# Performance work log

Measured on AMD Instinct MI355X. Metric: run time of the kernel, lower is better.

The kernel has to match this reference:

```python
import jax, jax.numpy as jnp
import numpy as np

B, N, ACHAN, VCHAN, H = 1, 2048, 128, 64, 8
KQ_ADIM, KQ_VDIM = 32, 16
AVALDIM, VVALDIM = ACHAN // H, VCHAN // H
KQ_PRESCALE, KQ_SCALE = 0.01, 0.1
R0_LIST = [0.5, 1.0, 2.0, 4.0, 0.5, 1.0, 2.0, 4.0]


def _init_w(key, shape, scale=1.0):
    # matches _param_init_with_scale: std = scale * fan_in**-0.5, shape (H, fan_in, fan_out)
    std = scale * shape[1] ** (-0.5)
    return std * jax.random.normal(key, shape, dtype=jnp.float32)


def setup_inputs() -> dict:
    key = jax.random.key(0)
    ks = jax.random.split(key, 12)
    kq_ascale = (KQ_PRESCALE / KQ_ADIM) ** 0.5
    kq_vscale = (KQ_PRESCALE / KQ_VDIM) ** 0.5
    return {
        "ax": jax.random.normal(ks[0], (B, N, ACHAN), jnp.float32),
        "vx": jax.random.normal(ks[1], (B, N, VCHAN, 3), jnp.float32),
        "pos_k": jax.random.normal(ks[2], (B, N, 3), jnp.float32),
        "pos_q": jax.random.normal(ks[3], (B, N, 3), jnp.float32),
        "r0": jnp.array(R0_LIST, jnp.float32),
        "W_ak": _init_w(ks[4], (H, KQ_ADIM, ACHAN), kq_ascale),
        "W_vk": _init_w(ks[5], (H, KQ_VDIM, VCHAN), kq_vscale),
        "W_aq": _init_w(ks[6], (H, KQ_ADIM, ACHAN), kq_ascale),
        "W_vq": _init_w(ks[7], (H, KQ_VDIM, VCHAN), kq_vscale),
        "W_aval": _init_w(ks[8], (H, AVALDIM, ACHAN)),
        "W_vval": _init_w(ks[9], (H, VVALDIM, VCHAN)),
        "W_a2vval": _init_w(ks[10], (H, VVALDIM, ACHAN)),
        "W_v2aval": _init_w(ks[11], (H, AVALDIM, VCHAN)),
    }


def reference(ax, vx, pos_k, pos_q, r0, W_ak, W_vk, W_aq, W_vq, W_aval, W_vval, W_a2vval, W_v2aval):
    batch, nodes, achan = ax.shape
    vchan = vx.shape[2]
    # key/query projections per head
    ak = jnp.einsum('hij,bnj->bnhi', W_ak, ax)      # (b,n,h,kq_adim)
    vk = jnp.einsum('hij,bnjv->bnhiv', W_vk, vx)    # (b,n,h,kq_vdim,3)
    aq = jnp.einsum('hij,bnj->bnhi', W_aq, ax)
    vq = jnp.einsum('hij,bnjv->bnhiv', W_vq, vx)
    akq_dot = jnp.einsum('bnhi,bmhi->bnmh', ak, aq)
    vkq_dot = jnp.einsum('bnhiv,bmhiv->bnmh', vk, vq)
    dot = KQ_SCALE * (akq_dot + vkq_dot)            # (b,n,m,h)
    # spatial proximity bias
    separation = pos_k[:, None, :, :] - pos_q[:, :, None, :]   # (b,n,m,3)
    dist_sq = jnp.sum(separation ** 2, axis=3)                 # (b,n,m)
    r0_sq = r0 ** 2
    proximity = r0_sq / (r0_sq + dist_sq[..., None])           # (b,n,m,h)
    directions = separation[:, :, :, None, :] * jnp.sqrt(proximity / r0_sq)[..., None]  # (b,n,m,h,3)
    attention = jax.nn.softmax(dot + jnp.log(proximity), axis=1)  # softmax over keys n
    # value mixing (project values per node first, then attend)
    aval = jnp.einsum('hij,bnj->bnhi', W_aval, ax)              # (b,n,h,avaldim)
    vval = jnp.einsum('hij,bnjv->bnhiv', W_vval, vx)            # (b,n,h,vvaldim,3)
    aans = jnp.einsum('bnmh,bnhi->bmhi', attention, aval)
    vans = jnp.einsum('bnmh,bnhiv->bmhiv', attention, vval)
    v2a = jnp.einsum('hij,bnjv->bnhiv', W_v2aval, vx)           # (b,n,h,avaldim,3)
    a2v = jnp.einsum('hij,bnj->bnhi', W_a2vval, ax)             # (b,n,h,vvaldim)
    aans = aans + jnp.einsum('bnmh,bnhiv,bnmhv->bmhi', attention, v2a, directions)
    vans = vans + jnp.einsum('bnmh,bnhi,bnmhv->bmhiv', attention, a2v, directions)
    return (aans.reshape(batch, nodes, achan), vans.reshape(batch, nodes, vchan, 3))
```

## Files before the change

### kernel.cpp

```cpp
#include <hip/hip_runtime.h>

#define NN 2048
#define NH 8

typedef __attribute__((ext_vector_type(4))) short s4;
typedef __attribute__((ext_vector_type(8))) short s8;
typedef __attribute__((ext_vector_type(4))) float f4;

static __device__ __forceinline__ ushort f2b(float x) {
    uint u = __builtin_bit_cast(uint, x);
    uint r = (u + 0x7FFFu + ((u >> 16) & 1u)) >> 16;
    return (ushort)r;
}
static __device__ __forceinline__ float b2f(ushort b) {
    return __builtin_bit_cast(float, ((uint)b) << 16);
}
static __device__ __forceinline__ uint pu(ushort a, ushort b) {
    return (uint)a | ((uint)b << 16);
}
static __device__ __forceinline__ s4 pack4(float a, float b, float c, float d) {
    uint2 w; w.x = pu(f2b(a), f2b(b)); w.y = pu(f2b(c), f2b(d));
    return __builtin_bit_cast(s4, w);
}
static __device__ __forceinline__ f4 mfma32(s8 a, s8 b, f4 c) {
    return __builtin_amdgcn_mfma_f32_16x16x32_bf16(a, b, c, 0, 0, 0);
}
static __device__ __forceinline__ f4 mfma16(s4 a, s4 b, f4 c) {
    const s4 z4s = {0, 0, 0, 0};
    s8 a8 = __builtin_shufflevector(a, z4s, 0, 1, 2, 3, 4, 5, 6, 7);
    s8 b8 = __builtin_shufflevector(b, z4s, 0, 1, 2, 3, 4, 5, 6, 7);
    return __builtin_amdgcn_mfma_f32_16x16x32_bf16(a8, b8, c, 0, 0, 0);
}

__global__ __launch_bounds__(256) void proj_kernel(
    const float* __restrict__ ax, const float* __restrict__ vx,
    const float* __restrict__ W_ak, const float* __restrict__ W_vk,
    const float* __restrict__ W_aq, const float* __restrict__ W_vq,
    const float* __restrict__ W_aval, const float* __restrict__ W_vval,
    const float* __restrict__ W_a2vval, const float* __restrict__ W_v2aval,
    ushort* __restrict__ Kf, ushort* __restrict__ Qf, ushort* __restrict__ Vn)
{
    __shared__ float axs[8][128];
    __shared__ float vxs[3][8][64];
    __shared__ __align__(16) ushort kqs[2][8][8][80];
    __shared__ __align__(16) ushort vns[8][8][152];
    const int t  = threadIdx.x;
    const int n0 = blockIdx.x * 8;

    for (int idx = t; idx < 8 * 128; idx += 256)
        axs[idx >> 7][idx & 127] = ax[n0 * 128 + idx];
    for (int idx = t; idx < 8 * 192; idx += 256) {
        int nb = idx / 192, r = idx - nb * 192;
        int j = r / 3, v = r - j * 3;
        vxs[v][nb][j] = vx[n0 * 192 + idx];
    }
    __syncthreads();

    #pragma unroll 1
    for (int rr = 0; rr < 8; ++rr) {
        int r = rr * 256 + t;
        const float* wrow; int h, v = 0, col = 0, vrow = -1, dsti = 0; bool isA;
        float scale = 1.0f;
        if (r < 256)       { int q = r;        h = q >> 5; wrow = W_ak     + q * 128;               isA = true;  dsti = 0; col = q & 31; }
        else if (r < 512)  { int q = r - 256;  h = q >> 5; wrow = W_aq     + q * 128;               isA = true;  dsti = 1; col = q & 31; scale = 0.1f; }
        else if (r < 896)  { int q = r - 512;  h = q / 48; int s = q - h * 48; v = s % 3; wrow = W_vk     + (h * 16 + s / 3) * 64; isA = false; dsti = 0; col = 32 + s; }
        else if (r < 1280) { int q = r - 896;  h = q / 48; int s = q - h * 48; v = s % 3; wrow = W_vq     + (h * 16 + s / 3) * 64; isA = false; dsti = 1; col = 32 + s; scale = 0.1f; }
        else if (r < 1408) { int q = r - 1280; h = q >> 4; wrow = W_aval   + q * 128;               isA = true;  vrow = q & 15; }
        else if (r < 1600) { int q = r - 1408; h = q / 24; int s = q - h * 24; v = s % 3; wrow = W_vval   + (h * 8  + s / 3) * 64; isA = false; vrow = 16 + s; }
        else if (r < 1984) { int q = r - 1600; h = q / 48; int s = q - h * 48; v = s % 3; wrow = W_v2aval + (h * 16 + s / 3) * 64; isA = false; vrow = 48 + s; }
        else               { int q = r - 1984; h = q >> 3; wrow = W_a2vval + q * 128;               isA = true;  vrow = 112 + (q & 7); }

        float acc[8] = {0.f, 0.f, 0.f, 0.f, 0.f, 0.f, 0.f, 0.f};
        if (isA) {
            for (int j = 0; j < 128; j += 4) {
                float4 w4 = *(const float4*)(wrow + j);
                #pragma unroll
                for (int nb = 0; nb < 8; ++nb) {
                    float4 x4 = *(const float4*)(&axs[nb][j]);
                    acc[nb] += w4.x * x4.x + w4.y * x4.y + w4.z * x4.z + w4.w * x4.w;
                }
            }
        } else {
            for (int j = 0; j < 64; j += 4) {
                float4 w4 = *(const float4*)(wrow + j);
                #pragma unroll
                for (int nb = 0; nb < 8; ++nb) {
                    float4 x4 = *(const float4*)(&vxs[v][nb][j]);
                    acc[nb] += w4.x * x4.x + w4.y * x4.y + w4.z * x4.z + w4.w * x4.w;
                }
            }
        }
        #pragma unroll
        for (int nb = 0; nb < 8; ++nb) {
            ushort bv = f2b(scale * acc[nb]);
            if (vrow >= 0) vns[h][nb][vrow] = bv;
            else           kqs[dsti][nb][h][col] = bv;
        }
    }
    __syncthreads();

    for (int i = t; i < 1280; i += 256) {
        int dsti = i / 640, rem = i - dsti * 640;
        int row = rem / 10, part = rem - row * 10;
        int h = row >> 3, nb = row & 7;
        uint4 val = *(const uint4*)(&kqs[dsti][nb][h][part * 8]);
        ushort* g = (dsti ? Qf : Kf) + ((size_t)h * NN + n0 + nb) * 128 + part * 8;
        *(uint4*)g = val;
    }
    for (int i = t; i < 1216; i += 256) {
        int row = i / 19, part = i - row * 19;
        int h = row >> 3, nb = row & 7;
        uint4 val = *(const uint4*)(&vns[h][nb][part * 8]);
        *(uint4*)(Vn + ((size_t)h * NN + n0 + nb) * 152 + part * 8) = val;
    }
}

__global__ __launch_bounds__(256) void finish_kernel(
    const float* __restrict__ pos_k, const float* __restrict__ pos_q,
    ushort* __restrict__ Kf, ushort* __restrict__ Qf)
{
    int g = blockIdx.x * 256 + threadIdx.x;
    int h = g >> 11, n = g & 2047;
    float pqx = pos_q[n * 3], pqy = pos_q[n * 3 + 1], pqz = pos_q[n * 3 + 2];
    float pkx = pos_k[n * 3], pky = pos_k[n * 3 + 1], pkz = pos_k[n * 3 + 2];

    ushort phx = f2b(pqx), phy = f2b(pqy), phz = f2b(pqz);
    float sq = pqx * pqx + pqy * pqy + pqz * pqz;
    ushort sqh = f2b(sq);
    ushort thx = f2b(pkx), thy = f2b(pky), thz = f2b(pkz);
    ushort qhx = f2b(-2.0f * b2f(thx)), qhy = f2b(-2.0f * b2f(thy)), qhz = f2b(-2.0f * b2f(thz));
    float sk = pkx * pkx + pky * pky + pkz * pkz;
    ushort skh = f2b(sk);

    uint4 z4; z4.x = 0; z4.y = 0; z4.z = 0; z4.w = 0;
    uint4 ka0, ka1;
    ka0.x = pu(phx, f2b(pqx - b2f(phx)));
    ka0.y = pu(phx, phy);
    ka0.z = pu(f2b(pqy - b2f(phy)), phy);
    ka0.w = pu(phz, f2b(pqz - b2f(phz)));
    ka1.x = pu(phz, sqh);
    ka1.y = pu(f2b(sq - b2f(sqh)), 0x3F80);
    ka1.z = pu(0x3F80, 0);
    ka1.w = 0;
    uint4 qa0, qa1;
    qa0.x = pu(qhx, qhx);
    qa0.y = pu(f2b(-2.0f * (pkx - b2f(thx))), qhy);
    qa0.z = pu(qhy, f2b(-2.0f * (pky - b2f(thy))));
    qa0.w = pu(qhz, qhz);
    qa1.x = pu(f2b(-2.0f * (pkz - b2f(thz))), 0x3F80);
    qa1.y = pu(0x3F80, skh);
    qa1.z = pu(f2b(sk - b2f(skh)), 0);
    qa1.w = 0;

    ushort* Ko = Kf + ((size_t)h * NN + n) * 128;
    ushort* Qo = Qf + ((size_t)h * NN + n) * 128;
    *(uint4*)(Ko + 80) = z4;  *(uint4*)(Ko + 88) = z4;
    *(uint4*)(Ko + 96) = ka0; *(uint4*)(Ko + 104) = ka1;
    *(uint4*)(Ko + 112) = z4; *(uint4*)(Ko + 120) = z4;
    *(uint4*)(Qo + 80) = z4;  *(uint4*)(Qo + 88) = z4;
    *(uint4*)(Qo + 96) = qa0; *(uint4*)(Qo + 104) = qa1;
    *(uint4*)(Qo + 112) = z4; *(uint4*)(Qo + 120) = z4;
}

__global__ __launch_bounds__(256) void vtrans_kernel(
    const ushort* __restrict__ Vn, const float* __restrict__ pos_q,
    ushort* __restrict__ Vt)
{
    __shared__ ushort lds_n[64 * 160];
    __shared__ float lds_pq[192];
    const int bid = blockIdx.x;
    const int h = bid & 7, n0 = (bid >> 3) * 64;
    const int t = threadIdx.x;

    const ushort* src = Vn + ((size_t)h * NN + n0) * 152;
    #pragma unroll
    for (int p = 0; p < 5; ++p) {
        int idx = p * 256 + t;
        if (idx < 1216) {
            int node = idx / 19, ch = idx - node * 19;
            *(uint4*)(&lds_n[node * 160 + ch * 8]) =
                *(const uint4*)(src + (size_t)node * 152 + ch * 8);
        }
    }
    if (t < 192) lds_pq[t] = pos_q[n0 * 3 + t];
    __syncthreads();

    #pragma unroll 1
    for (int p = 0; p < 5; ++p) {
        int fi = p * 32 + (t >> 3);
        if (fi < 144) {
            int nb0 = (t & 7) * 8;
            uint rr[4];
            #pragma unroll
            for (int e = 0; e < 8; ++e) {
                int node = nb0 + e;
                const ushort* row = lds_n + node * 160;
                ushort bv;
                if (fi < 40 || (fi >= 48 && fi < 96) || (fi >= 112 && fi < 120)) {
                    bv = row[fi];
                } else if (fi < 48) {
                    bv = (fi == 40) ? (ushort)0x3F80 : (ushort)0;
                } else if (fi < 112) {
                    int i = fi - 96;
                    float val = b2f(row[48 + 3 * i]) * lds_pq[node * 3 + 0]
                              + b2f(row[49 + 3 * i]) * lds_pq[node * 3 + 1]
                              + b2f(row[50 + 3 * i]) * lds_pq[node * 3 + 2];
                    bv = f2b(val);
                } else {
                    int s = fi - 120, ip = s / 3, v = s - 3 * ip;
                    bv = f2b(b2f(row[112 + ip]) * lds_pq[node * 3 + v]);
                }
                if ((e & 1) == 0) rr[e >> 1] = bv;
                else              rr[e >> 1] |= ((uint)bv) << 16;
            }
            uint4 outw; outw.x = rr[0]; outw.y = rr[1]; outw.z = rr[2]; outw.w = rr[3];
            *(uint4*)(Vt + ((size_t)h * 144 + fi) * NN + n0 + nb0) = outw;
        }
    }
}

__global__ __launch_bounds__(256, 2) void attn_kernel(
    const ushort* __restrict__ Kf, const ushort* __restrict__ Qf,
    const ushort* __restrict__ Vt, const float* __restrict__ pos_k,
    const float* __restrict__ r0, float* __restrict__ out)
{
    __shared__ __align__(16) char smem[39168];
    const int bid = blockIdx.x;
    const int h = bid & 7;
    const int m0 = (bid >> 3) * 32;
    const int t = threadIdx.x;
    const int lane = t & 63, w = t >> 6;
    const int l15 = lane & 15, lg = lane >> 4;
    const int kh = w >> 1, qh = w & 1;

    const float r0h = r0[h], r0sq = r0h * r0h;
    const ushort* Kg = Kf + (size_t)h * NN * 128;
    const ushort* Vg = Vt + (size_t)h * 144 * NN;

    const ushort* Qp = Qf + ((size_t)h * NN + m0 + qh * 16 + l15) * 128 + lg * 8;
    const s8 qb0 = *(const s8*)(Qp);
    const s8 qb1 = *(const s8*)(Qp + 32);
    const s8 qb2 = *(const s8*)(Qp + 64);
    const s8 qb3 = *(const s8*)(Qp + 96);

    f4 acc[9];
    #pragma unroll
    for (int jb = 0; jb < 9; ++jb) acc[jb] = (f4){0.f, 0.f, 0.f, 0.f};

    uint4 kreg0, kreg1, vreg0, vreg1, vreg2;
    const int kt = t >> 4, kgr = t & 15;
    const int vf = t >> 2, vg = t & 3;
    const int kc = kgr * 8;
    const int vc = vg * 8;
    const int kS = (((kgr & 8) | ((kgr + kt) & 7))) << 4;
    const int kws0 = kt * 256 + kS;
    const int kws1 = kws0 + 4096;
    const int vS = ((vg + (vf >> 1)) & 3) << 4;
    const int vws0 = vf * 64 + vS;
    const int vws1 = vws0 + 4096;
    const int vws2 = vws0 + 8192;

    const int kro = (kh * 16 + l15) * 256;
    const int e0 = ((lg + l15) & 7) << 4;
    const int e1 = ((lg + l15 + 4) & 7) << 4;
    const int vxo = (((kh * 2 + (lg >> 1) + (l15 >> 1)) & 3) << 4) + ((lg & 1) << 3);

#define LOAD_TILE(k0)                                                               \
    kreg0 = *(const uint4*)(Kg + (size_t)((k0) + kt) * 128 + kc);                   \
    kreg1 = *(const uint4*)(Kg + (size_t)((k0) + 16 + kt) * 128 + kc);              \
    vreg0 = *(const uint4*)(Vg + (size_t)vf * NN + (k0) + vc);                      \
    vreg1 = *(const uint4*)(Vg + (size_t)(vf + 64) * NN + (k0) + vc);               \
    if (t < 64) vreg2 = *(const uint4*)(Vg + (size_t)(vf + 128) * NN + (k0) + vc);

#define WRITE_TILE(b)                                                               \
  { char* kb_ = smem + (b) * 17408; char* vb_ = kb_ + 8192;                         \
    *(uint4*)(kb_ + kws0) = kreg0;  *(uint4*)(kb_ + kws1) = kreg1;                  \
    *(uint4*)(vb_ + vws0) = vreg0;  *(uint4*)(vb_ + vws1) = vreg1;                  \
    if (t < 64) *(uint4*)(vb_ + vws2) = vreg2; }

#define COMPUTE_TILE(b)                                                             \
  { const char* kb_ = smem + (b) * 17408; const char* vb_ = kb_ + 8192;             \
    const char* kr = kb_ + kro;                                                     \
    s8 ka0 = *(const s8*)(kr + e0);                                                 \
    s8 ka1 = *(const s8*)(kr + e1);                                                 \
    s8 ka2 = *(const s8*)(kr + 128 + e0);                                           \
    s8 ka3 = *(const s8*)(kr + 128 + e1);                                           \
    f4 z = (f4){0.f, 0.f, 0.f, 0.f};                                                \
    f4 dt = mfma32(ka0, qb0, z);                                                    \
    dt = mfma32(ka1, qb1, dt);                                                      \
    dt = mfma32(ka2, qb2, dt);                                                      \
    f4 dd = mfma32(ka3, qb3, z);                                                    \
    float pv[4], gv[4];                                                             \
    _Pragma("unroll")                                                               \
    for (int r = 0; r < 4; ++r) {                                                   \
      float x = r0sq + dd[r];                                                       \
      float rs = __builtin_amdgcn_rsqf(x);                                          \
      float tt = rs * rs;                                                           \
      float y = dt[r];                                                              \
      float e = fmaf(y, fmaf(0.5f, y, 1.0f), 1.0f);                                 \
      pv[r] = r0sq * tt * e;                                                        \
      gv[r] = pv[r] * rs;                                                           \
    }                                                                               \
    s4 pb = pack4(pv[0], pv[1], pv[2], pv[3]);                                      \
    s4 gb = pack4(gv[0], gv[1], gv[2], gv[3]);                                      \
    const char* vr = vb_ + l15 * 64 + vxo;                                          \
    _Pragma("unroll")                                                               \
    for (int jb = 0; jb < 3; ++jb)                                                  \
      acc[jb] = mfma16(*(const s4*)(vr + jb * 1024), pb, acc[jb]);                  \
    _Pragma("unroll")                                                               \
    for (int jb = 3; jb < 9; ++jb)                                                  \
      acc[jb] = mfma16(*(const s4*)(vr + jb * 1024), gb, acc[jb]);                  \
  }

    LOAD_TILE(0)
    WRITE_TILE(0)
    __syncthreads();
    #pragma unroll 2
    for (int tile = 0; tile < 64; ++tile) {
        int b = tile & 1;
        if (tile < 63) { LOAD_TILE((tile + 1) * 32) }
        COMPUTE_TILE(b)
        __syncthreads();
        if (tile < 63) { WRITE_TILE(b ^ 1) }
        __syncthreads();
    }

    float* smemf = (float*)smem;
    float my[36];
    #pragma unroll
    for (int jb = 0; jb < 9; ++jb)
        #pragma unroll
        for (int r = 0; r < 4; ++r)
            my[jb * 4 + r] = acc[jb][r];

    if (w >= 2) {
        float* p = smemf + ((w - 2) * 64 + lane) * 37;
        #pragma unroll
        for (int i = 0; i < 36; ++i) p[i] = my[i];
    }
    __syncthreads();
    if (w < 2) {
        const float* p = smemf + (w * 64 + lane) * 37;
        #pragma unroll
        for (int i = 0; i < 36; ++i) my[i] += p[i];
    }
    __syncthreads();
    if (w < 2) {
        #pragma unroll
        for (int jb = 0; jb < 9; ++jb)
            #pragma unroll
            for (int r = 0; r < 4; ++r)
                smemf[((size_t)w * 144 + jb * 16 + lg * 4 + r) * 17 + l15]
                    = my[jb * 4 + r];
    }
    __syncthreads();

    {
        int q = t & 31, task = t >> 5;
        int m = m0 + q, qh2 = q >> 4, ml = q & 15;
        const float* R = smemf + (size_t)qh2 * 144 * 17 + ml;
        float inv = 1.0f / R[40 * 17];
        float pk0 = pos_k[m * 3], pk1 = pos_k[m * 3 + 1], pk2 = pos_k[m * 3 + 2];
        #pragma unroll
        for (int oo = 0; oo < 5; ++oo) {
            int o = task * 5 + oo;
            if (o < 16) {
                int i = o;
                float val = R[i * 17] + pk0 * R[(48 + 3 * i) * 17] + pk1 * R[(49 + 3 * i) * 17]
                          + pk2 * R[(50 + 3 * i) * 17] - R[(96 + i) * 17];
                out[(size_t)m * 128 + h * 16 + i] = val * inv;
            } else {
                int s = o - 16, ip = s / 3, v3 = s - 3 * ip;
                float pkv = (v3 == 0) ? pk0 : ((v3 == 1) ? pk1 : pk2);
                float val = R[(16 + s) * 17] + pkv * R[(112 + ip) * 17] - R[(120 + s) * 17];
                out[(size_t)NN * 128 + (size_t)m * 192 + h * 24 + s] = val * inv;
            }
        }
    }
#undef LOAD_TILE
#undef WRITE_TILE
#undef COMPUTE_TILE
}

extern "C" void kernel_launch(void* const* d_in, const int* in_sizes, int n_in,
                              void* d_out, int out_size, void* d_ws, size_t ws_size,
                              hipStream_t stream) {
    const float* ax       = (const float*)d_in[0];
    const float* vx       = (const float*)d_in[1];
    const float* pos_k    = (const float*)d_in[2];
    const float* pos_q    = (const float*)d_in[3];
    const float* r0       = (const float*)d_in[4];
    const float* W_ak     = (const float*)d_in[5];
    const float* W_vk     = (const float*)d_in[6];
    const float* W_aq     = (const float*)d_in[7];
    const float* W_vq     = (const float*)d_in[8];
    const float* W_aval   = (const float*)d_in[9];
    const float* W_vval   = (const float*)d_in[10];
    const float* W_a2vval = (const float*)d_in[11];
    const float* W_v2aval = (const float*)d_in[12];

    ushort* Kf = (ushort*)d_ws;
    ushort* Qf = Kf + (size_t)NH * NN * 128;
    ushort* Vn = Qf + (size_t)NH * NN * 128;
    ushort* Vt = Vn + (size_t)NH * NN * 152;
    float*  outp = (float*)d_out;

    hipLaunchKernelGGL(proj_kernel, dim3(NN / 8), dim3(256), 0, stream,
                       ax, vx, W_ak, W_vk, W_aq, W_vq, W_aval, W_vval,
                       W_a2vval, W_v2aval, Kf, Qf, Vn);
    hipLaunchKernelGGL(finish_kernel, dim3(64), dim3(256), 0, stream,
                       pos_k, pos_q, Kf, Qf);
    hipLaunchKernelGGL(vtrans_kernel, dim3(32 * NH), dim3(256), 0, stream,
                       Vn, pos_q, Vt);
    hipLaunchKernelGGL(attn_kernel, dim3(64 * NH), dim3(256), 0, stream,
                       Kf, Qf, Vt, pos_k, r0, outp);
}
```

Baseline: 111.5 us.

## Fuse position finish and value transpose into projection kernel

Merges finish_kernel and vtrans_kernel into proj_kernel, so four launches become two. The value rows are now written directly in the transposed Vt layout. The position-weighted terms are computed from a pos_q-contracted vx in shared memory and from scaled a2v rows, which removes the Vn intermediate buffer and its round trip through global memory. The block size doubles to 512 threads. The projection does slightly more work (2368 rows instead of 2048), and each thread writes 16-byte chunks strided across Vt rows.

```diff
diff --git a/kernel.cpp b/kernel.cpp
--- a/kernel.cpp
+++ b/kernel.cpp
@@ -18,8 +18,11 @@
 static __device__ __forceinline__ uint pu(ushort a, ushort b) {
     return (uint)a | ((uint)b << 16);
 }
+static __device__ __forceinline__ uint bpack(float lo, float hi) {
+    return pu(f2b(lo), f2b(hi));
+}
 static __device__ __forceinline__ s4 pack4(float a, float b, float c, float d) {
-    uint2 w; w.x = pu(f2b(a), f2b(b)); w.y = pu(f2b(c), f2b(d));
+    uint2 w; w.x = bpack(a, b); w.y = bpack(c, d);
     return __builtin_bit_cast(s4, w);
 }
 static __device__ __forceinline__ f4 mfma32(s8 a, s8 b, f4 c) {
@@ -32,46 +35,58 @@
     return __builtin_amdgcn_mfma_f32_16x16x32_bf16(a8, b8, c, 0, 0, 0);
 }
 
-__global__ __launch_bounds__(256) void proj_kernel(
+__global__ __launch_bounds__(512) void proj_kernel(
     const float* __restrict__ ax, const float* __restrict__ vx,
+    const float* __restrict__ pos_k, const float* __restrict__ pos_q,
     const float* __restrict__ W_ak, const float* __restrict__ W_vk,
     const float* __restrict__ W_aq, const float* __restrict__ W_vq,
     const float* __restrict__ W_aval, const float* __restrict__ W_vval,
     const float* __restrict__ W_a2vval, const float* __restrict__ W_v2aval,
-    ushort* __restrict__ Kf, ushort* __restrict__ Qf, ushort* __restrict__ Vn)
+    ushort* __restrict__ Kf, ushort* __restrict__ Qf, ushort* __restrict__ Vt)
 {
     __shared__ float axs[8][128];
     __shared__ float vxs[3][8][64];
+    __shared__ float xts[8][64];
+    __shared__ float pqs[8][3];
     __shared__ __align__(16) ushort kqs[2][8][8][80];
-    __shared__ __align__(16) ushort vns[8][8][152];
     const int t  = threadIdx.x;
     const int n0 = blockIdx.x * 8;
 
-    for (int idx = t; idx < 8 * 128; idx += 256)
+    for (int idx = t; idx < 1024; idx += 512)
         axs[idx >> 7][idx & 127] = ax[n0 * 128 + idx];
-    for (int idx = t; idx < 8 * 192; idx += 256) {
+    for (int idx = t; idx < 1536; idx += 512) {
         int nb = idx / 192, r = idx - nb * 192;
         int j = r / 3, v = r - j * 3;
         vxs[v][nb][j] = vx[n0 * 192 + idx];
     }
+    if (t < 24) pqs[t / 3][t % 3] = pos_q[n0 * 3 + t];
+    __syncthreads();
+    {
+        int nb = t >> 6, j = t & 63;
+        xts[nb][j] = vxs[0][nb][j] * pqs[nb][0] + vxs[1][nb][j] * pqs[nb][1]
+                   + vxs[2][nb][j] * pqs[nb][2];
+    }
     __syncthreads();
 
     #pragma unroll 1
-    for (int rr = 0; rr < 8; ++rr) {
-        int r = rr * 256 + t;
-        const float* wrow; int h, v = 0, col = 0, vrow = -1, dsti = 0; bool isA;
+    for (int rr = 0; rr < 5; ++rr) {
+        int r = rr * 512 + t;
+        if (r >= 2368) continue;
+        const float* wrow; int h, v = 0, col = -1, vrow = -1, dsti = 0, srcT = 0, pv = -1;
         float scale = 1.0f;
-        if (r < 256)       { int q = r;        h = q >> 5; wrow = W_ak     + q * 128;               isA = true;  dsti = 0; col = q & 31; }
-        else if (r < 512)  { int q = r - 256;  h = q >> 5; wrow = W_aq     + q * 128;               isA = true;  dsti = 1; col = q & 31; scale = 0.1f; }
-        else if (r < 896)  { int q = r - 512;  h = q / 48; int s = q - h * 48; v = s % 3; wrow = W_vk     + (h * 16 + s / 3) * 64; isA = false; dsti = 0; col = 32 + s; }
-        else if (r < 1280) { int q = r - 896;  h = q / 48; int s = q - h * 48; v = s % 3; wrow = W_vq     + (h * 16 + s / 3) * 64; isA = false; dsti = 1; col = 32 + s; scale = 0.1f; }
-        else if (r < 1408) { int q = r - 1280; h = q >> 4; wrow = W_aval   + q * 128;               isA = true;  vrow = q & 15; }
-        else if (r < 1600) { int q = r - 1408; h = q / 24; int s = q - h * 24; v = s % 3; wrow = W_vval   + (h * 8  + s / 3) * 64; isA = false; vrow = 16 + s; }
-        else if (r < 1984) { int q = r - 1600; h = q / 48; int s = q - h * 48; v = s % 3; wrow = W_v2aval + (h * 16 + s / 3) * 64; isA = false; vrow = 48 + s; }
-        else               { int q = r - 1984; h = q >> 3; wrow = W_a2vval + q * 128;               isA = true;  vrow = 112 + (q & 7); }
+        if (r < 256)       { int q = r;        h = q >> 5; wrow = W_ak + q * 128; srcT = 0; col = q & 31; dsti = 0; }
+        else if (r < 512)  { int q = r - 256;  h = q >> 5; wrow = W_aq + q * 128; srcT = 0; col = q & 31; dsti = 1; scale = 0.1f; }
+        else if (r < 896)  { int q = r - 512;  h = q / 48; int s = q - h * 48; v = s % 3; wrow = W_vk + (h * 16 + s / 3) * 64; srcT = 1; col = 32 + s; dsti = 0; }
+        else if (r < 1280) { int q = r - 896;  h = q / 48; int s = q - h * 48; v = s % 3; wrow = W_vq + (h * 16 + s / 3) * 64; srcT = 1; col = 32 + s; dsti = 1; scale = 0.1f; }
+        else if (r < 1408) { int q = r - 1280; h = q >> 4; wrow = W_aval + q * 128; srcT = 0; vrow = q & 15; }
+        else if (r < 1600) { int q = r - 1408; h = q / 24; int s = q - h * 24; v = s % 3; wrow = W_vval + (h * 8 + s / 3) * 64; srcT = 1; vrow = 16 + s; }
+        else if (r < 1984) { int q = r - 1600; h = q / 48; int s = q - h * 48; v = s % 3; wrow = W_v2aval + (h * 16 + s / 3) * 64; srcT = 1; vrow = 48 + s; }
+        else if (r < 2048) { int q = r - 1984; h = q >> 3; wrow = W_a2vval + q * 128; srcT = 0; vrow = 112 + (q & 7); }
+        else if (r < 2176) { int q = r - 2048; h = q >> 4; wrow = W_v2aval + (h * 16 + (q & 15)) * 64; srcT = 2; vrow = 96 + (q & 15); }
+        else               { int q = r - 2176; h = q / 24; int s = q - h * 24; int i = s / 3; pv = s % 3; wrow = W_a2vval + (h * 8 + i) * 128; srcT = 0; vrow = 120 + s; }
 
         float acc[8] = {0.f, 0.f, 0.f, 0.f, 0.f, 0.f, 0.f, 0.f};
-        if (isA) {
+        if (srcT == 0) {
             for (int j = 0; j < 128; j += 4) {
                 float4 w4 = *(const float4*)(wrow + j);
                 #pragma unroll
@@ -81,25 +96,34 @@
                 }
             }
         } else {
+            const float* sp = (srcT == 1) ? &vxs[v][0][0] : &xts[0][0];
             for (int j = 0; j < 64; j += 4) {
                 float4 w4 = *(const float4*)(wrow + j);
                 #pragma unroll
                 for (int nb = 0; nb < 8; ++nb) {
-                    float4 x4 = *(const float4*)(&vxs[v][nb][j]);
+                    float4 x4 = *(const float4*)(sp + nb * 64 + j);
                     acc[nb] += w4.x * x4.x + w4.y * x4.y + w4.z * x4.z + w4.w * x4.w;
                 }
             }
         }
-        #pragma unroll
-        for (int nb = 0; nb < 8; ++nb) {
-            ushort bv = f2b(scale * acc[nb]);
-            if (vrow >= 0) vns[h][nb][vrow] = bv;
-            else           kqs[dsti][nb][h][col] = bv;
+        if (vrow >= 0) {
+            float o[8];
+            #pragma unroll
+            for (int nb = 0; nb < 8; ++nb)
+                o[nb] = acc[nb] * (pv >= 0 ? pqs[nb][pv] : 1.0f);
+            uint4 pk;
+            pk.x = bpack(o[0], o[1]); pk.y = bpack(o[2], o[3]);
+            pk.z = bpack(o[4], o[5]); pk.w = bpack(o[6], o[7]);
+            *(uint4*)(Vt + ((size_t)(h * 144 + vrow)) * NN + n0) = pk;
+        } else {
+            #pragma unroll
+            for (int nb = 0; nb < 8; ++nb)
+                kqs[dsti][nb][h][col] = f2b(scale * acc[nb]);
         }
     }
     __syncthreads();
 
-    for (int i = t; i < 1280; i += 256) {
+    for (int i = t; i < 1280; i += 512) {
         int dsti = i / 640, rem = i - dsti * 640;
         int row = rem / 10, part = rem - row * 10;
         int h = row >> 3, nb = row & 7;
@@ -107,115 +131,54 @@
         ushort* g = (dsti ? Qf : Kf) + ((size_t)h * NN + n0 + nb) * 128 + part * 8;
         *(uint4*)g = val;
     }
-    for (int i = t; i < 1216; i += 256) {
-        int row = i / 19, part = i - row * 19;
-        int h = row >> 3, nb = row & 7;
-        uint4 val = *(const uint4*)(&vns[h][nb][part * 8]);
-        *(uint4*)(Vn + ((size_t)h * NN + n0 + nb) * 152 + part * 8) = val;
-    }
-}
-
-__global__ __launch_bounds__(256) void finish_kernel(
-    const float* __restrict__ pos_k, const float* __restrict__ pos_q,
-    ushort* __restrict__ Kf, ushort* __restrict__ Qf)
-{
-    int g = blockIdx.x * 256 + threadIdx.x;
-    int h = g >> 11, n = g & 2047;
-    float pqx = pos_q[n * 3], pqy = pos_q[n * 3 + 1], pqz = pos_q[n * 3 + 2];
-    float pkx = pos_k[n * 3], pky = pos_k[n * 3 + 1], pkz = pos_k[n * 3 + 2];
-
-    ushort phx = f2b(pqx), phy = f2b(pqy), phz = f2b(pqz);
-    float sq = pqx * pqx + pqy * pqy + pqz * pqz;
-    ushort sqh = f2b(sq);
-    ushort thx = f2b(pkx), thy = f2b(pky), thz = f2b(pkz);
-    ushort qhx = f2b(-2.0f * b2f(thx)), qhy = f2b(-2.0f * b2f(thy)), qhz = f2b(-2.0f * b2f(thz));
-    float sk = pkx * pkx + pky * pky + pkz * pkz;
-    ushort skh = f2b(sk);
-
-    uint4 z4; z4.x = 0; z4.y = 0; z4.z = 0; z4.w = 0;
-    uint4 ka0, ka1;
-    ka0.x = pu(phx, f2b(pqx - b2f(phx)));
-    ka0.y = pu(phx, phy);
-    ka0.z = pu(f2b(pqy - b2f(phy)), phy);
-    ka0.w = pu(phz, f2b(pqz - b2f(phz)));
-    ka1.x = pu(phz, sqh);
-    ka1.y = pu(f2b(sq - b2f(sqh)), 0x3F80);
-    ka1.z = pu(0x3F80, 0);
-    ka1.w = 0;
-    uint4 qa0, qa1;
-    qa0.x = pu(qhx, qhx);
-    qa0.y = pu(f2b(-2.0f * (pkx - b2f(thx))), qhy);
-    qa0.z = pu(qhy, f2b(-2.0f * (pky - b2f(thy))));
-    qa0.w = pu(qhz, qhz);
-    qa1.x = pu(f2b(-2.0f * (pkz - b2f(thz))), 0x3F80);
-    qa1.y = pu(0x3F80, skh);
-    qa1.z = pu(f2b(sk - b2f(skh)), 0);
-    qa1.w = 0;
-
-    ushort* Ko = Kf + ((size_t)h * NN + n) * 128;
-    ushort* Qo = Qf + ((size_t)h * NN + n) * 128;
-    *(uint4*)(Ko + 80) = z4;  *(uint4*)(Ko + 88) = z4;
-    *(uint4*)(Ko + 96) = ka0; *(uint4*)(Ko + 104) = ka1;
-    *(uint4*)(Ko + 112) = z4; *(uint4*)(Ko + 120) = z4;
-    *(uint4*)(Qo + 80) = z4;  *(uint4*)(Qo + 88) = z4;
-    *(uint4*)(Qo + 96) = qa0; *(uint4*)(Qo + 104) = qa1;
-    *(uint4*)(Qo + 112) = z4; *(uint4*)(Qo + 120) = z4;
-}
-
-__global__ __launch_bounds__(256) void vtrans_kernel(
-    const ushort* __restrict__ Vn, const float* __restrict__ pos_q,
-    ushort* __restrict__ Vt)
-{
-    __shared__ ushort lds_n[64 * 160];
-    __shared__ float lds_pq[192];
-    const int bid = blockIdx.x;
-    const int h = bid & 7, n0 = (bid >> 3) * 64;
-    const int t = threadIdx.x;
-
-    const ushort* src = Vn + ((size_t)h * NN + n0) * 152;
-    #pragma unroll
-    for (int p = 0; p < 5; ++p) {
-        int idx = p * 256 + t;
-        if (idx < 1216) {
-            int node = idx / 19, ch = idx - node * 19;
-            *(uint4*)(&lds_n[node * 160 + ch * 8]) =
-                *(const uint4*)(src + (size_t)node * 152 + ch * 8);
-        }
-    }
-    if (t < 192) lds_pq[t] = pos_q[n0 * 3 + t];
-    __syncthreads();
-
-    #pragma unroll 1
-    for (int p = 0; p < 5; ++p) {
-        int fi = p * 32 + (t >> 3);
-        if (fi < 144) {
-            int nb0 = (t & 7) * 8;
-            uint rr[4];
-            #pragma unroll
-            for (int e = 0; e < 8; ++e) {
-                int node = nb0 + e;
-                const ushort* row = lds_n + node * 160;
-                ushort bv;
-                if (fi < 40 || (fi >= 48 && fi < 96) || (fi >= 112 && fi < 120)) {
-                    bv = row[fi];
-                } else if (fi < 48) {
-                    bv = (fi == 40) ? (ushort)0x3F80 : (ushort)0;
-                } else if (fi < 112) {
-                    int i = fi - 96;
-                    float val = b2f(row[48 + 3 * i]) * lds_pq[node * 3 + 0]
-                              + b2f(row[49 + 3 * i]) * lds_pq[node * 3 + 1]
-                              + b2f(row[50 + 3 * i]) * lds_pq[node * 3 + 2];
-                    bv = f2b(val);
-                } else {
-                    int s = fi - 120, ip = s / 3, v = s - 3 * ip;
-                    bv = f2b(b2f(row[112 + ip]) * lds_pq[node * 3 + v]);
-                }
-                if ((e & 1) == 0) rr[e >> 1] = bv;
-                else              rr[e >> 1] |= ((uint)bv) << 16;
-            }
-            uint4 outw; outw.x = rr[0]; outw.y = rr[1]; outw.z = rr[2]; outw.w = rr[3];
-            *(uint4*)(Vt + ((size_t)h * 144 + fi) * NN + n0 + nb0) = outw;
-        }
+
+    if (t < 64) {
+        int h = t >> 3, nb = t & 7, n = n0 + nb;
+        float pqx = pqs[nb][0], pqy = pqs[nb][1], pqz = pqs[nb][2];
+        float pkx = pos_k[n * 3], pky = pos_k[n * 3 + 1], pkz = pos_k[n * 3 + 2];
+
+        ushort phx = f2b(pqx), phy = f2b(pqy), phz = f2b(pqz);
+        float sq = pqx * pqx + pqy * pqy + pqz * pqz;
+        ushort sqh = f2b(sq);
+        ushort thx = f2b(pkx), thy = f2b(pky), thz = f2b(pkz);
+        ushort qhx = f2b(-2.0f * b2f(thx)), qhy = f2b(-2.0f * b2f(thy)), qhz = f2b(-2.0f * b2f(thz));
+        float sk = pkx * pkx + pky * pky + pkz * pkz;
+        ushort skh = f2b(sk);
+
+        uint4 z4; z4.x = 0; z4.y = 0; z4.z = 0; z4.w = 0;
+        uint4 ka0, ka1;
+        ka0.x = pu(phx, f2b(pqx - b2f(phx)));
+        ka0.y = pu(phx, phy);
+        ka0.z = pu(f2b(pqy - b2f(phy)), phy);
+        ka0.w = pu(phz, f2b(pqz - b2f(phz)));
+        ka1.x = pu(phz, sqh);
+        ka1.y = pu(f2b(sq - b2f(sqh)), 0x3F80);
+        ka1.z = pu(0x3F80, 0);
+        ka1.w = 0;
+        uint4 qa0, qa1;
+        qa0.x = pu(qhx, qhx);
+        qa0.y = pu(f2b(-2.0f * (pkx - b2f(thx))), qhy);
+        qa0.z = pu(qhy, f2b(-2.0f * (pky - b2f(thy))));
+        qa0.w = pu(qhz, qhz);
+        qa1.x = pu(f2b(-2.0f * (pkz - b2f(thz))), 0x3F80);
+        qa1.y = pu(0x3F80, skh);
+        qa1.z = pu(f2b(sk - b2f(skh)), 0);
+        qa1.w = 0;
+
+        ushort* Ko = Kf + ((size_t)h * NN + n) * 128;
+        ushort* Qo = Qf + ((size_t)h * NN + n) * 128;
+        *(uint4*)(Ko + 80) = z4;  *(uint4*)(Ko + 88) = z4;
+        *(uint4*)(Ko + 96) = ka0; *(uint4*)(Ko + 104) = ka1;
+        *(uint4*)(Ko + 112) = z4; *(uint4*)(Ko + 120) = z4;
+        *(uint4*)(Qo + 80) = z4;  *(uint4*)(Qo + 88) = z4;
+        *(uint4*)(Qo + 96) = qa0; *(uint4*)(Qo + 104) = qa1;
+        *(uint4*)(Qo + 112) = z4; *(uint4*)(Qo + 120) = z4;
+    } else if (t < 128) {
+        int idx = t - 64, h = idx >> 3, rw = 40 + (idx & 7);
+        uint4 cv;
+        if (rw == 40) { cv.x = 0x3F803F80u; cv.y = 0x3F803F80u; cv.z = 0x3F803F80u; cv.w = 0x3F803F80u; }
+        else          { cv.x = 0; cv.y = 0; cv.z = 0; cv.w = 0; }
+        *(uint4*)(Vt + ((size_t)(h * 144 + rw)) * NN + n0) = cv;
     }
 }
 
@@ -401,17 +364,12 @@
 
     ushort* Kf = (ushort*)d_ws;
     ushort* Qf = Kf + (size_t)NH * NN * 128;
-    ushort* Vn = Qf + (size_t)NH * NN * 128;
-    ushort* Vt = Vn + (size_t)NH * NN * 152;
+    ushort* Vt = Qf + (size_t)NH * NN * 128;
     float*  outp = (float*)d_out;
 
-    hipLaunchKernelGGL(proj_kernel, dim3(NN / 8), dim3(256), 0, stream,
-                       ax, vx, W_ak, W_vk, W_aq, W_vq, W_aval, W_vval,
-                       W_a2vval, W_v2aval, Kf, Qf, Vn);
-    hipLaunchKernelGGL(finish_kernel, dim3(64), dim3(256), 0, stream,
-                       pos_k, pos_q, Kf, Qf);
-    hipLaunchKernelGGL(vtrans_kernel, dim3(32 * NH), dim3(256), 0, stream,
-                       Vn, pos_q, Vt);
+    hipLaunchKernelGGL(proj_kernel, dim3(NN / 8), dim3(512), 0, stream,
+                       ax, vx, pos_k, pos_q, W_ak, W_vk, W_aq, W_vq,
+                       W_aval, W_vval, W_a2vval, W_v2aval, Kf, Qf, Vt);
     hipLaunchKernelGGL(attn_kernel, dim3(64 * NH), dim3(256), 0, stream,
                        Kf, Qf, Vt, pos_k, r0, outp);
 }
```

Measured after the change: 104.7 us. -6.1%, faster.
